# Kernel optimization log

Measured on AMD Instinct MI355X. Metric: run time of the kernel, lower is better.

Reference implementation:

```python
import jax, jax.numpy as jnp
import numpy as np

B, S, D = 4, 2048, 1024
NH = 16
H2 = NH // 2
F = D // NH  # per-head hidden = 64
EXP = 4
DECAY_CONST = S // 512  # 4
EPS = 1e-5


def setup_inputs() -> dict:
    key = jax.random.key(0)
    ks = jax.random.split(key, 8)
    inp = {
        "x": jax.random.normal(ks[0], (B, S, D), dtype=jnp.float32),
        # token_norm / channel_norm params (LayerNorm init: ones/zeros)
        "g1": jnp.ones((D,), jnp.float32), "b1": jnp.zeros((D,), jnp.float32),
        "g2": jnp.ones((D,), jnp.float32), "b2": jnp.zeros((D,), jnp.float32),
        # per-head input projections [NH, D, F] and output projection
        "Wp": jax.random.normal(ks[1], (NH, D, F), jnp.float32) * 0.02,
        "bp": jnp.zeros((NH, F), jnp.float32),
        "Wo": jax.random.normal(ks[2], (D, D), jnp.float32) * 0.02,
        "bo": jnp.zeros((D,), jnp.float32),
        # ColRepeatCausalLinear: weight = 0.4, bias = 3 ; RowRepeat: -0.3, 0.2
        "w_col": jnp.full((H2, S), 0.4, jnp.float32),
        "b_col": jnp.full((H2, S), 3.0, jnp.float32),
        "w_row": jnp.full((H2, S), -0.3, jnp.float32),
        "b_row": jnp.full((H2, S), 0.2, jnp.float32),
        # decay_value params (ones, clipped to [0.9, 1] then ** (1/decay_constant))
        "dcol": jnp.ones((H2,), jnp.float32),
        "drow": jnp.ones((H2,), jnp.float32),
        # channel MLP
        "W1": jax.random.normal(ks[3], (D, EXP * D), jnp.float32) * 0.02,
        "c1": jnp.zeros((EXP * D,), jnp.float32),
        "W2": jax.random.normal(ks[4], (EXP * D, D), jnp.float32) * 0.02,
        "c2": jnp.zeros((D,), jnp.float32),
    }
    return inp


def _ln(x, g, b):
    m = jnp.mean(x, axis=-1, keepdims=True)
    v = jnp.mean(jnp.square(x - m), axis=-1, keepdims=True)
    return (x - m) * jax.lax.rsqrt(v + EPS) * g + b


def _forward(x, g1, b1, g2, b2, Wp, bp, Wo, bo, w_col, b_col, w_row, b_row,
             dcol, drow, W1, c1, W2, c2):
    decay_c = jnp.clip(dcol, 0.9, 1.0) ** (1.0 / DECAY_CONST)  # [H2]
    decay_r = jnp.clip(drow, 0.9, 1.0) ** (1.0 / DECAY_CONST)  # [H2]

    def step(carry, inp):
        cc, rc = carry                      # each [B, H2, F]
        xt, wc, bc, wr, br = inp            # xt [B, D]; wc/bc/wr/br [H2]
        # token mixing branch
        h = _ln(xt, g1, b1)
        proj = jnp.einsum('bd,hdf->bhf', h, Wp) + bp  # [B, NH, F]
        # Col heads: cache = proj + decay*cache ; out = w*cache + b
        cc = proj[:, :H2] + decay_c[None, :, None] * cc
        col_out = wc[None, :, None] * cc + bc[None, :, None]
        # Row heads: cache = w*proj + decay*cache ; out = cache + b
        rc = wr[None, :, None] * proj[:, H2:] + decay_r[None, :, None] * rc
        row_out = rc + br[None, :, None]
        mix = jnp.concatenate([col_out, row_out], axis=1).reshape(xt.shape[0], -1)
        y = xt + mix @ Wo + bo
        # channel MLP branch
        h2 = _ln(y, g2, b2)
        out = y + jax.nn.gelu(h2 @ W1 + c1) @ W2 + c2
        return (cc, rc), out

    init = (jnp.zeros((x.shape[0], H2, F), x.dtype),
            jnp.zeros((x.shape[0], H2, F), x.dtype))
    xs = (jnp.swapaxes(x, 0, 1), w_col.T, b_col.T, w_row.T, b_row.T)
    _, ys = jax.lax.scan(step, init, xs)    # ys [S, B, D]
    return jnp.swapaxes(ys, 0, 1)


def reference(x, g1, b1, g2, b2, Wp, bp, Wo, bo, w_col, b_col, w_row, b_row,
              dcol, drow, W1, c1, W2, c2):
    return _forward(x, g1, b1, g2, b2, Wp, bp, Wo, bo, w_col, b_col,
                    w_row, b_row, dcol, drow, W1, c1, W2, c2)
```

## Files before the change

kernel.cpp:

```cpp
#include <hip/hip_runtime.h>

typedef __attribute__((ext_vector_type(4))) float fx4;
typedef __attribute__((ext_vector_type(8))) short s16x8;

#define SEQ   2048
#define DM    1024
#define BSZ   4
#define ROWS  (BSZ*SEQ)
#define CHUNK 64
#define NCH   (SEQ/CHUNK)

__device__ __forceinline__ unsigned short f2bf(float f){
  unsigned u = __builtin_bit_cast(unsigned, f);
  u = u + 0x7FFFu + ((u >> 16) & 1u);
  return (unsigned short)(u >> 16);
}
__device__ __forceinline__ float bf2f(unsigned short u){
  return __builtin_bit_cast(float, ((unsigned)u) << 16);
}

__device__ __forceinline__ float gelu_f(float x){
  float u = 0.7978845608028654f * (x + 0.044715f * x*x*x);
  return x / (1.0f + __expf(-2.0f*u));
}

__device__ __forceinline__ void gload_lds16(const void* g, void* l){
  __builtin_amdgcn_global_load_lds(
      (__attribute__((address_space(1))) void*)g,
      (__attribute__((address_space(3))) void*)l, 16, 0, 0);
}

__global__ __launch_bounds__(256) void transpose_k(const float* __restrict__ in,
    unsigned short* __restrict__ out, int R, int C, long long ibs, long long obs){
  __shared__ float tile[32][33];
  in  += (long long)blockIdx.z * ibs;
  out += (long long)blockIdx.z * obs;
  int c0 = blockIdx.x*32, r0 = blockIdx.y*32;
  int tx = threadIdx.x, ty = threadIdx.y;
  #pragma unroll
  for (int i=0;i<4;i++)
    tile[ty+8*i][tx] = in[(long long)(r0+ty+8*i)*C + c0+tx];
  __syncthreads();
  #pragma unroll
  for (int i=0;i<4;i++)
    out[(long long)(c0+ty+8*i)*R + r0+tx] = f2bf(tile[tx][ty+8*i]);
}

__global__ __launch_bounds__(256) void ln_rows(const float* __restrict__ x,
    const float* __restrict__ g, const float* __restrict__ b,
    unsigned short* __restrict__ out){
  int row = blockIdx.x, t = threadIdx.x;
  const fx4* xr = (const fx4*)(x + (long long)row*DM);
  fx4 v = xr[t];
  float s  = v[0]+v[1]+v[2]+v[3];
  float s2 = v[0]*v[0]+v[1]*v[1]+v[2]*v[2]+v[3]*v[3];
  #pragma unroll
  for (int o=32;o;o>>=1){ s += __shfl_down(s,o); s2 += __shfl_down(s2,o); }
  __shared__ float red[8];
  int lane = t & 63, wid = t >> 6;
  if (lane==0){ red[wid]=s; red[4+wid]=s2; }
  __syncthreads();
  s  = red[0]+red[1]+red[2]+red[3];
  s2 = red[4]+red[5]+red[6]+red[7];
  float m  = s * (1.0f/DM);
  float rs = rsqrtf(s2*(1.0f/DM) - m*m + 1e-5f);
  const fx4 gv = ((const fx4*)g)[t], bv = ((const fx4*)b)[t];
  ushort4 pk;
  pk.x = f2bf((v[0]-m)*rs*gv[0] + bv[0]);
  pk.y = f2bf((v[1]-m)*rs*gv[1] + bv[1]);
  pk.z = f2bf((v[2]-m)*rs*gv[2] + bv[2]);
  pk.w = f2bf((v[3]-m)*rs*gv[3] + bv[3]);
  *(ushort4*)(out + (long long)row*DM + t*4) = pk;
}

__global__ __launch_bounds__(256) void scan_carry(const unsigned short* __restrict__ P,
    const float* __restrict__ w_row, const float* __restrict__ dcol,
    const float* __restrict__ drow, float* __restrict__ carry){
  int g = blockIdx.x*4 + (threadIdx.x>>6);
  int lane = threadIdx.x & 63;
  int chunk = g & (NCH-1); int bh = g >> 5; int h = bh & 15; int b = bh >> 4;
  float draw = (h<8) ? dcol[h] : drow[h-8];
  float d = powf(fminf(fmaxf(draw,0.9f),1.0f), 0.25f);
  float c = 0.f;
  const unsigned short* p = P + ((long long)(b*SEQ + chunk*CHUNK))*DM + h*64 + lane;
  const float* wr = w_row + (h>=8 ? (h-8)*SEQ + chunk*CHUNK : 0);
  #pragma unroll 4
  for (int i=0;i<CHUNK;i++){
    float a = bf2f(p[(long long)i*DM]);
    if (h>=8) a *= wr[i];
    c = fmaf(d, c, a);
  }
  carry[((long long)(bh*64 + lane))*NCH + chunk] = c;
}

__global__ __launch_bounds__(256) void scan_final(const unsigned short* __restrict__ P,
    const float* __restrict__ w_col, const float* __restrict__ b_col,
    const float* __restrict__ w_row, const float* __restrict__ b_row,
    const float* __restrict__ dcol, const float* __restrict__ drow,
    const float* __restrict__ carry, unsigned short* __restrict__ mix){
  int g = blockIdx.x*4 + (threadIdx.x>>6);
  int lane = threadIdx.x & 63;
  int chunk = g & (NCH-1); int bh = g >> 5; int h = bh & 15; int b = bh >> 4;
  float draw = (h<8) ? dcol[h] : drow[h-8];
  float d = powf(fminf(fmaxf(draw,0.9f),1.0f), 0.25f);
  float dL = d;
  #pragma unroll
  for (int i=0;i<6;i++) dL *= dL;
  const float* cr = carry + ((long long)(bh*64 + lane))*NCH;
  float c = 0.f;
  for (int j=0;j<chunk;j++) c = fmaf(dL, c, cr[j]);
  const unsigned short* p = P + ((long long)(b*SEQ + chunk*CHUNK))*DM + h*64 + lane;
  unsigned short* mo = mix + ((long long)(b*SEQ + chunk*CHUNK))*DM + h*64 + lane;
  int t0 = chunk*CHUNK;
  #pragma unroll 4
  for (int i=0;i<CHUNK;i++){
    int t = t0 + i;
    float a = bf2f(p[(long long)i*DM]);
    float o;
    if (h<8){
      c = fmaf(d, c, a);
      o = w_col[h*SEQ + t]*c + b_col[h*SEQ + t];
    } else {
      a *= w_row[(h-8)*SEQ + t];
      c = fmaf(d, c, a);
      o = c + b_row[(h-8)*SEQ + t];
    }
    mo[(long long)i*DM] = f2bf(o);
  }
}

template<int EPI, int K>
__global__ __launch_bounds__(256) void gemm_bt(const unsigned short* __restrict__ A,
    const unsigned short* __restrict__ Bt, int N,
    const float* __restrict__ bias, const float* __restrict__ res,
    float* __restrict__ outf, unsigned short* __restrict__ outb){
  __shared__ __align__(16) unsigned short lds[32768];
  const int tid = threadIdx.x;
  const int l = tid & 63;
  const int w = tid >> 6;
  const int wr = w >> 1, wc = w & 1;

  const long long row0 = (long long)blockIdx.x * 128;
  const long long col0 = (long long)blockIdx.y * 128;

  fx4 acc[4][4] = {};

  const unsigned short* gA[4];
  const unsigned short* gB[4];
  int lslot[4];
  #pragma unroll
  for (int i=0;i<4;i++){
    int slot = w*256 + i*64 + l;
    int r = slot >> 3;
    int qs = slot & 7;
    int c = (qs ^ (r & 7)) << 3;
    gA[i] = A  + (row0 + r)*(long long)K + c;
    gB[i] = Bt + (col0 + r)*(long long)K + c;
    lslot[i] = slot*8;
  }
  int aoff[2][4], boff[2][4];
  #pragma unroll
  for (int kk=0;kk<2;kk++){
    #pragma unroll
    for (int m=0;m<4;m++){
      int r  = wr*64 + m*16 + (l&15);
      int q  = (kk*4 + (l>>4)) ^ (r&7);
      aoff[kk][m] = r*64 + q*8;
      int r2 = wc*64 + m*16 + (l&15);
      int q2 = (kk*4 + (l>>4)) ^ (r2&7);
      boff[kk][m] = 8192 + r2*64 + q2*8;
    }
  }

  auto STAGE = [&](int bufoff){
    #pragma unroll
    for (int i=0;i<4;i++){
      gload_lds16(gA[i], &lds[bufoff + lslot[i]]);
      gload_lds16(gB[i], &lds[bufoff + 8192 + lslot[i]]);
      gA[i] += 64; gB[i] += 64;
    }
  };

  constexpr int nsteps = K >> 6;

  STAGE(0);
  STAGE(16384);
  asm volatile("s_waitcnt vmcnt(8)" ::: "memory");
  __builtin_amdgcn_sched_barrier(0);
  __builtin_amdgcn_s_barrier();

  int curoff = 0;
  for (int s = 0; s < nsteps; ++s){
    s16x8 af[2][4], bfr[2][4];
    #pragma unroll
    for (int kk=0;kk<2;kk++){
      #pragma unroll
      for (int m=0;m<4;m++){
        af[kk][m]  = *(const s16x8*)&lds[curoff + aoff[kk][m]];
        bfr[kk][m] = *(const s16x8*)&lds[curoff + boff[kk][m]];
      }
    }
    __builtin_amdgcn_sched_barrier(0);
    asm volatile("s_waitcnt lgkmcnt(0)" ::: "memory");
    __builtin_amdgcn_sched_barrier(0);
    __builtin_amdgcn_s_barrier();
    __builtin_amdgcn_sched_barrier(0);
    const bool do_stage = (s + 2 < nsteps);
    if (do_stage) STAGE(curoff);
    __builtin_amdgcn_s_setprio(1);
    #pragma unroll
    for (int kk=0;kk<2;kk++)
      #pragma unroll
      for (int m=0;m<4;m++)
        #pragma unroll
        for (int n=0;n<4;n++)
          acc[m][n] = __builtin_amdgcn_mfma_f32_16x16x32_bf16(af[kk][m], bfr[kk][n], acc[m][n], 0, 0, 0);
    __builtin_amdgcn_s_setprio(0);
    if (s + 1 < nsteps){
      __builtin_amdgcn_sched_barrier(0);
      if (do_stage) asm volatile("s_waitcnt vmcnt(8)" ::: "memory");
      else          asm volatile("s_waitcnt vmcnt(0)" ::: "memory");
      __builtin_amdgcn_sched_barrier(0);
      __builtin_amdgcn_s_barrier();
      __builtin_amdgcn_sched_barrier(0);
    }
    curoff ^= 16384;
  }
  __syncthreads();

  float* lf = (float*)lds;
  const int lg = l >> 4, lc = l & 15;
  #pragma unroll
  for (int g=0; g<4; ++g){
    if (wr == (g>>1)){
      #pragma unroll
      for (int mm=0; mm<2; ++mm){
        const int m = (g&1)*2 + mm;
        int lrow = mm*16 + lg*4;
        #pragma unroll
        for (int n=0;n<4;n++){
          int col = wc*64 + n*16 + lc;
          #pragma unroll
          for (int rg=0;rg<4;rg++)
            lf[(lrow+rg)*132 + col] = acc[m][n][rg];
        }
      }
    }
    __syncthreads();
    #pragma unroll
    for (int j=0;j<4;j++){
      int flat = j*256 + tid;
      int lrow = flat >> 5, c4 = flat & 31;
      long long grow = row0 + g*32 + lrow;
      long long gcol = col0 + c4*4;
      fx4 v = *(fx4*)&lf[lrow*132 + c4*4];
      fx4 bv = *(const fx4*)&bias[gcol];
      v = v + bv;
      long long idx = grow*(long long)N + gcol;
      if constexpr (EPI==0){
        *(fx4*)&outf[idx] = v;
      } else if constexpr (EPI==1){
        fx4 rv = *(const fx4*)&res[idx];
        v = v + rv;
        *(fx4*)&outf[idx] = v;
      } else if constexpr (EPI==2){
        ushort4 pk;
        pk.x = f2bf(gelu_f(v[0]));
        pk.y = f2bf(gelu_f(v[1]));
        pk.z = f2bf(gelu_f(v[2]));
        pk.w = f2bf(gelu_f(v[3]));
        *(ushort4*)&outb[idx] = pk;
      } else {
        ushort4 pk;
        pk.x = f2bf(v[0]); pk.y = f2bf(v[1]);
        pk.z = f2bf(v[2]); pk.w = f2bf(v[3]);
        *(ushort4*)&outb[idx] = pk;
      }
    }
    __syncthreads();
  }
}

extern "C" void kernel_launch(void* const* d_in, const int* in_sizes, int n_in,
                              void* d_out, int out_size, void* d_ws, size_t ws_size,
                              hipStream_t stream){
  const float* x    = (const float*)d_in[0];
  const float* g1   = (const float*)d_in[1];
  const float* b1   = (const float*)d_in[2];
  const float* g2   = (const float*)d_in[3];
  const float* b2   = (const float*)d_in[4];
  const float* Wp   = (const float*)d_in[5];
  const float* bp   = (const float*)d_in[6];
  const float* Wo   = (const float*)d_in[7];
  const float* bo   = (const float*)d_in[8];
  const float* w_col= (const float*)d_in[9];
  const float* b_col= (const float*)d_in[10];
  const float* w_row= (const float*)d_in[11];
  const float* b_row= (const float*)d_in[12];
  const float* dcol = (const float*)d_in[13];
  const float* drow = (const float*)d_in[14];
  const float* W1   = (const float*)d_in[15];
  const float* c1   = (const float*)d_in[16];
  const float* W2   = (const float*)d_in[17];
  const float* c2   = (const float*)d_in[18];
  float* out = (float*)d_out;

  char* ws = (char*)d_ws;
  const size_t MB = 1024*1024;
  if (ws_size < 101*MB) return;
  unsigned short* Wpt = (unsigned short*)(ws + 0);
  unsigned short* Wot = (unsigned short*)(ws + 2*MB);
  unsigned short* W1t = (unsigned short*)(ws + 4*MB);
  unsigned short* W2t = (unsigned short*)(ws + 12*MB);
  unsigned short* h   = (unsigned short*)(ws + 20*MB);
  unsigned short* P   = (unsigned short*)(ws + 36*MB);
  unsigned short* mix = (unsigned short*)(ws + 68*MB);
  float*          carry=(float*)(ws + 84*MB);
  unsigned short* U   = (unsigned short*)(ws + 36*MB);
  unsigned short* yln = h;

  dim3 tb(32,8);
  transpose_k<<<dim3(2,32,16),  tb, 0, stream>>>(Wp, Wpt, 1024,   64, 65536LL, 65536LL);
  transpose_k<<<dim3(32,32,1),  tb, 0, stream>>>(Wo, Wot, 1024, 1024, 0LL, 0LL);
  transpose_k<<<dim3(128,32,1), tb, 0, stream>>>(W1, W1t, 1024, 4096, 0LL, 0LL);
  transpose_k<<<dim3(32,128,1), tb, 0, stream>>>(W2, W2t, 4096, 1024, 0LL, 0LL);

  ln_rows<<<dim3(ROWS), dim3(256), 0, stream>>>(x, g1, b1, h);
  gemm_bt<3,1024><<<dim3(64,8),  dim3(256), 0, stream>>>(h,   Wpt, 1024, bp, nullptr, nullptr, P);
  scan_carry<<<dim3(512), dim3(256), 0, stream>>>(P, w_row, dcol, drow, carry);
  scan_final<<<dim3(512), dim3(256), 0, stream>>>(P, w_col, b_col, w_row, b_row, dcol, drow, carry, mix);
  gemm_bt<1,1024><<<dim3(64,8),  dim3(256), 0, stream>>>(mix, Wot, 1024, bo, x, out, nullptr);
  ln_rows<<<dim3(ROWS), dim3(256), 0, stream>>>(out, g2, b2, yln);
  gemm_bt<2,1024><<<dim3(64,32), dim3(256), 0, stream>>>(yln, W1t, 4096, c1, nullptr, nullptr, U);
  gemm_bt<1,4096><<<dim3(64,8),  dim3(256), 0, stream>>>(U,   W2t, 1024, c2, out, out, nullptr);
}
```

Measured before the change: 311.7 us.

## Add 256x256-tile 8-wave GEMM with phased LDS pipeline for W1 projection

Introduces a new GEMM kernel with 256x256 output tiles, 512 threads and 128KB of double-buffered LDS. Each k-step is split into four phases that interleave the next stage's global-to-LDS loads with MFMA work, with s_setprio raised around the MFMAs. The epilogue stages results through LDS for coalesced stores. It is used only for the 8192x4096 W1 GEMM with fused GELU. The larger tiles raise arithmetic intensity per block, but only 512 blocks run at one block per CU, so occupancy drops.

```diff
diff --git a/kernel.cpp b/kernel.cpp
--- a/kernel.cpp
+++ b/kernel.cpp
@@ -139,7 +139,6 @@
   const int l = tid & 63;
   const int w = tid >> 6;
   const int wr = w >> 1, wc = w & 1;
-
   const long long row0 = (long long)blockIdx.x * 128;
   const long long col0 = (long long)blockIdx.y * 128;
 
@@ -171,7 +170,6 @@
       boff[kk][m] = 8192 + r2*64 + q2*8;
     }
   }
-
   auto STAGE = [&](int bufoff){
     #pragma unroll
     for (int i=0;i<4;i++){
@@ -180,9 +178,7 @@
       gA[i] += 64; gB[i] += 64;
     }
   };
-
   constexpr int nsteps = K >> 6;
-
   STAGE(0);
   STAGE(16384);
   asm volatile("s_waitcnt vmcnt(8)" ::: "memory");
@@ -281,6 +277,154 @@
   }
 }
 
+#define PH(M0, N0, STG, LASTW)                                                \
+  {                                                                           \
+    s16x8 afr[2][4], bfr[2][2];                                               \
+    _Pragma("unroll")                                                         \
+    for (int kk=0;kk<2;kk++){                                                 \
+      _Pragma("unroll")                                                       \
+      for (int i=0;i<4;i++)                                                   \
+        afr[kk][i] = *(const s16x8*)&lds[bufb + aBase + qa[kk] + (M0+i)*1024];\
+      _Pragma("unroll")                                                       \
+      for (int j=0;j<2;j++)                                                   \
+        bfr[kk][j] = *(const s16x8*)&lds[bufb + bBase + qb[kk] + (N0+j)*1024];\
+    }                                                                         \
+    __builtin_amdgcn_sched_barrier(0);                                        \
+    STG;                                                                      \
+    __builtin_amdgcn_sched_barrier(0);                                        \
+    __builtin_amdgcn_s_barrier();                                             \
+    asm volatile("s_waitcnt lgkmcnt(0)" ::: "memory");                        \
+    __builtin_amdgcn_sched_barrier(0);                                        \
+    __builtin_amdgcn_s_setprio(1);                                            \
+    _Pragma("unroll")                                                         \
+    for (int kk=0;kk<2;kk++)                                                  \
+      _Pragma("unroll")                                                       \
+      for (int i=0;i<4;i++)                                                   \
+        _Pragma("unroll")                                                     \
+        for (int j=0;j<2;j++)                                                 \
+          acc[M0+i][N0+j] = __builtin_amdgcn_mfma_f32_16x16x32_bf16(          \
+              afr[kk][i], bfr[kk][j], acc[M0+i][N0+j], 0, 0, 0);              \
+    __builtin_amdgcn_s_setprio(0);                                            \
+    __builtin_amdgcn_sched_barrier(0);                                        \
+    LASTW;                                                                    \
+    __builtin_amdgcn_s_barrier();                                             \
+    __builtin_amdgcn_sched_barrier(0);                                        \
+  }
+
+template<int EPI, int K>
+__global__ __launch_bounds__(512) void gemm256(const unsigned short* __restrict__ A,
+    const unsigned short* __restrict__ Bt, int N,
+    const float* __restrict__ bias, const float* __restrict__ res,
+    float* __restrict__ outf, unsigned short* __restrict__ outb){
+  __shared__ __align__(16) unsigned short lds[65536];
+  const int tid = threadIdx.x;
+  const int l = tid & 63;
+  const int w = tid >> 6;
+  const int wr = w >> 2;
+  const int wcn = w & 3;
+  const long long row0 = (long long)blockIdx.x * 256;
+  const long long col0 = (long long)blockIdx.y * 256;
+
+  fx4 acc[8][4] = {};
+
+  const unsigned short* gA[4];
+  const unsigned short* gB[4];
+  int lsl[4];
+  #pragma unroll
+  for (int i=0;i<4;i++){
+    int slot = i*512 + tid;
+    int r = slot >> 3, q = slot & 7;
+    int c = (q ^ (r & 7)) << 3;
+    gA[i] = A  + (row0 + r)*(long long)K + c;
+    gB[i] = Bt + (col0 + r)*(long long)K + c;
+    lsl[i] = slot*8;
+  }
+  const int l15 = l & 15, lg = l >> 4;
+  const int aRow = wr*128 + l15;
+  const int bRow = wcn*64 + l15;
+  const int qa[2] = { ((lg    ) ^ (aRow & 7))*8, ((4+lg) ^ (aRow & 7))*8 };
+  const int qb[2] = { ((lg    ) ^ (bRow & 7))*8, ((4+lg) ^ (bRow & 7))*8 };
+  const int aBase = aRow*64;
+  const int bBase = 16384 + bRow*64;
+
+  auto STAGE_A = [&](int nb){
+    #pragma unroll
+    for (int i=0;i<4;i++){ gload_lds16(gA[i], &lds[nb + lsl[i]]); gA[i] += 64; }
+  };
+  auto STAGE_B = [&](int nb){
+    #pragma unroll
+    for (int i=0;i<4;i++){ gload_lds16(gB[i], &lds[nb + 16384 + lsl[i]]); gB[i] += 64; }
+  };
+
+  constexpr int T = K >> 6;
+  STAGE_A(0); STAGE_B(0);
+  asm volatile("s_waitcnt vmcnt(0)" ::: "memory");
+  __builtin_amdgcn_sched_barrier(0);
+  __builtin_amdgcn_s_barrier();
+
+  int bufb = 0;
+  for (int t = 0; t < T; ++t){
+    const int nb = bufb ^ 32768;
+    const bool more = (t + 1 < T);
+    PH(0,0, { if (more) STAGE_A(nb); }, {});
+    PH(4,0, { if (more) STAGE_B(nb); }, {});
+    PH(0,2, {}, {});
+    PH(4,2, {}, { if (more) asm volatile("s_waitcnt vmcnt(0)" ::: "memory"); });
+    bufb = nb;
+  }
+
+  float* lf = (float*)lds;
+  #pragma unroll
+  for (int g=0; g<4; ++g){
+    if (wr == (g>>1)){
+      #pragma unroll
+      for (int mm=0; mm<4; ++mm){
+        const int m = (g&1)*4 + mm;
+        const int lrow = mm*16 + lg*4;
+        #pragma unroll
+        for (int n=0;n<4;n++){
+          const int col = wcn*64 + n*16 + l15;
+          #pragma unroll
+          for (int rg=0;rg<4;rg++)
+            lf[(lrow+rg)*260 + col] = acc[m][n][rg];
+        }
+      }
+    }
+    __syncthreads();
+    #pragma unroll
+    for (int j=0;j<8;j++){
+      int flat = j*512 + tid;
+      int lrow = flat >> 6, c4 = flat & 63;
+      long long grow = row0 + g*64 + lrow;
+      long long gcol = col0 + c4*4;
+      fx4 v = *(fx4*)&lf[lrow*260 + c4*4];
+      fx4 bv = *(const fx4*)&bias[gcol];
+      v = v + bv;
+      long long idx = grow*(long long)N + gcol;
+      if constexpr (EPI==0){
+        *(fx4*)&outf[idx] = v;
+      } else if constexpr (EPI==1){
+        fx4 rv = *(const fx4*)&res[idx];
+        v = v + rv;
+        *(fx4*)&outf[idx] = v;
+      } else if constexpr (EPI==2){
+        ushort4 pk;
+        pk.x = f2bf(gelu_f(v[0]));
+        pk.y = f2bf(gelu_f(v[1]));
+        pk.z = f2bf(gelu_f(v[2]));
+        pk.w = f2bf(gelu_f(v[3]));
+        *(ushort4*)&outb[idx] = pk;
+      } else {
+        ushort4 pk;
+        pk.x = f2bf(v[0]); pk.y = f2bf(v[1]);
+        pk.z = f2bf(v[2]); pk.w = f2bf(v[3]);
+        *(ushort4*)&outb[idx] = pk;
+      }
+    }
+    __syncthreads();
+  }
+}
+
 extern "C" void kernel_launch(void* const* d_in, const int* in_sizes, int n_in,
                               void* d_out, int out_size, void* d_ws, size_t ws_size,
                               hipStream_t stream){
@@ -331,6 +475,6 @@
   scan_final<<<dim3(512), dim3(256), 0, stream>>>(P, w_col, b_col, w_row, b_row, dcol, drow, carry, mix);
   gemm_bt<1,1024><<<dim3(64,8),  dim3(256), 0, stream>>>(mix, Wot, 1024, bo, x, out, nullptr);
   ln_rows<<<dim3(ROWS), dim3(256), 0, stream>>>(out, g2, b2, yln);
-  gemm_bt<2,1024><<<dim3(64,32), dim3(256), 0, stream>>>(yln, W1t, 4096, c1, nullptr, nullptr, U);
+  gemm256<2,1024><<<dim3(32,16), dim3(512), 0, stream>>>(yln, W1t, 4096, c1, nullptr, nullptr, U);
   gemm_bt<1,4096><<<dim3(64,8),  dim3(256), 0, stream>>>(U,   W2t, 1024, c2, out, out, nullptr);
 }
```

New measurement: 312.9 us. About the same (+0.4%).

## Run channel MLP GEMMs in FP8 with MX-scaled MFMA

Applied to the files above, without the earlier changes.

Converts W1/W2 weights (scaled by 64) and the LN2 output plus GELU intermediate to FP8 E4M3. The two MLP GEMMs, which dominate FLOPs, then run on a new kernel using 16x16x128 scaled MFMA with fixed exponent scales to undo the weight scaling. This halves operand bytes and uses the higher-throughput FP8 matrix path. The cost is reduced precision, with a risk of accuracy tolerance failure.

```diff
diff --git a/kernel.cpp b/kernel.cpp
--- a/kernel.cpp
+++ b/kernel.cpp
@@ -2,6 +2,8 @@
 
 typedef __attribute__((ext_vector_type(4))) float fx4;
 typedef __attribute__((ext_vector_type(8))) short s16x8;
+typedef __attribute__((ext_vector_type(4))) int   i32x4;
+typedef __attribute__((ext_vector_type(8))) int   i32x8;
 
 #define SEQ   2048
 #define DM    1024
@@ -19,6 +21,22 @@
   return __builtin_bit_cast(float, ((unsigned)u) << 16);
 }
 
+__device__ __forceinline__ unsigned char f2fp8(float x){
+  unsigned u = __builtin_bit_cast(unsigned, x);
+  unsigned s = (u >> 24) & 0x80u;
+  float ax = __builtin_fabsf(x);
+  if (ax >= 448.f) return (unsigned char)(s | 0x7Eu);
+  if (ax < 0.015625f){
+    int m = (int)(ax * 512.f + 0.5f);
+    return (unsigned char)(s | (unsigned)m);
+  }
+  unsigned b = __builtin_bit_cast(unsigned, ax);
+  b += 0x0007FFFFu + ((b >> 20) & 1u);
+  unsigned e = (b >> 23) - 127u + 7u;
+  unsigned m = (b >> 20) & 7u;
+  return (unsigned char)(s | (e << 3) | m);
+}
+
 __device__ __forceinline__ float gelu_f(float x){
   float u = 0.7978845608028654f * (x + 0.044715f * x*x*x);
   return x / (1.0f + __expf(-2.0f*u));
@@ -28,6 +46,12 @@
   __builtin_amdgcn_global_load_lds(
       (__attribute__((address_space(1))) void*)g,
       (__attribute__((address_space(3))) void*)l, 16, 0, 0);
+}
+
+__device__ __forceinline__ fx4 mfma_mx(i32x8 a, i32x8 b, fx4 c){
+  return __builtin_amdgcn_mfma_scale_f32_16x16x128_f8f6f4(
+      a, b, c, 0 , 0 ,
+      0, 0x7F7F7F7F, 0, 0x79797979);
 }
 
 __global__ __launch_bounds__(256) void transpose_k(const float* __restrict__ in,
@@ -44,6 +68,20 @@
   #pragma unroll
   for (int i=0;i<4;i++)
     out[(long long)(c0+ty+8*i)*R + r0+tx] = f2bf(tile[tx][ty+8*i]);
+}
+
+__global__ __launch_bounds__(256) void transpose_f8(const float* __restrict__ in,
+    unsigned char* __restrict__ out, int R, int C){
+  __shared__ float tile[32][33];
+  int c0 = blockIdx.x*32, r0 = blockIdx.y*32;
+  int tx = threadIdx.x, ty = threadIdx.y;
+  #pragma unroll
+  for (int i=0;i<4;i++)
+    tile[ty+8*i][tx] = in[(long long)(r0+ty+8*i)*C + c0+tx];
+  __syncthreads();
+  #pragma unroll
+  for (int i=0;i<4;i++)
+    out[(long long)(c0+ty+8*i)*R + r0+tx] = f2fp8(tile[tx][ty+8*i] * 64.f);
 }
 
 __global__ __launch_bounds__(256) void ln_rows(const float* __restrict__ x,
@@ -71,6 +109,33 @@
   pk.z = f2bf((v[2]-m)*rs*gv[2] + bv[2]);
   pk.w = f2bf((v[3]-m)*rs*gv[3] + bv[3]);
   *(ushort4*)(out + (long long)row*DM + t*4) = pk;
+}
+
+__global__ __launch_bounds__(256) void ln_rows_f8(const float* __restrict__ x,
+    const float* __restrict__ g, const float* __restrict__ b,
+    unsigned char* __restrict__ out){
+  int row = blockIdx.x, t = threadIdx.x;
+  const fx4* xr = (const fx4*)(x + (long long)row*DM);
+  fx4 v = xr[t];
+  float s  = v[0]+v[1]+v[2]+v[3];
+  float s2 = v[0]*v[0]+v[1]*v[1]+v[2]*v[2]+v[3]*v[3];
+  #pragma unroll
+  for (int o=32;o;o>>=1){ s += __shfl_down(s,o); s2 += __shfl_down(s2,o); }
+  __shared__ float red[8];
+  int lane = t & 63, wid = t >> 6;
+  if (lane==0){ red[wid]=s; red[4+wid]=s2; }
+  __syncthreads();
+  s  = red[0]+red[1]+red[2]+red[3];
+  s2 = red[4]+red[5]+red[6]+red[7];
+  float m  = s * (1.0f/DM);
+  float rs = rsqrtf(s2*(1.0f/DM) - m*m + 1e-5f);
+  const fx4 gv = ((const fx4*)g)[t], bv = ((const fx4*)b)[t];
+  uchar4 pk;
+  pk.x = f2fp8((v[0]-m)*rs*gv[0] + bv[0]);
+  pk.y = f2fp8((v[1]-m)*rs*gv[1] + bv[1]);
+  pk.z = f2fp8((v[2]-m)*rs*gv[2] + bv[2]);
+  pk.w = f2fp8((v[3]-m)*rs*gv[3] + bv[3]);
+  *(uchar4*)(out + (long long)row*DM + t*4) = pk;
 }
 
 __global__ __launch_bounds__(256) void scan_carry(const unsigned short* __restrict__ P,
@@ -139,7 +204,6 @@
   const int l = tid & 63;
   const int w = tid >> 6;
   const int wr = w >> 1, wc = w & 1;
-
   const long long row0 = (long long)blockIdx.x * 128;
   const long long col0 = (long long)blockIdx.y * 128;
 
@@ -171,7 +235,6 @@
       boff[kk][m] = 8192 + r2*64 + q2*8;
     }
   }
-
   auto STAGE = [&](int bufoff){
     #pragma unroll
     for (int i=0;i<4;i++){
@@ -180,9 +243,7 @@
       gA[i] += 64; gB[i] += 64;
     }
   };
-
   constexpr int nsteps = K >> 6;
-
   STAGE(0);
   STAGE(16384);
   asm volatile("s_waitcnt vmcnt(8)" ::: "memory");
@@ -263,18 +324,153 @@
         fx4 rv = *(const fx4*)&res[idx];
         v = v + rv;
         *(fx4*)&outf[idx] = v;
-      } else if constexpr (EPI==2){
-        ushort4 pk;
-        pk.x = f2bf(gelu_f(v[0]));
-        pk.y = f2bf(gelu_f(v[1]));
-        pk.z = f2bf(gelu_f(v[2]));
-        pk.w = f2bf(gelu_f(v[3]));
-        *(ushort4*)&outb[idx] = pk;
       } else {
         ushort4 pk;
         pk.x = f2bf(v[0]); pk.y = f2bf(v[1]);
         pk.z = f2bf(v[2]); pk.w = f2bf(v[3]);
         *(ushort4*)&outb[idx] = pk;
+      }
+    }
+    __syncthreads();
+  }
+}
+
+template<int EPI, int K>
+__global__ __launch_bounds__(256) void gemm_f8(const unsigned char* __restrict__ A,
+    const unsigned char* __restrict__ Bt, int N,
+    const float* __restrict__ bias, const float* __restrict__ res,
+    float* __restrict__ outf, unsigned char* __restrict__ outb){
+  __shared__ __align__(16) unsigned char lds[65536];
+  const int tid = threadIdx.x;
+  const int l = tid & 63;
+  const int w = tid >> 6;
+  const int wr = w >> 1, wc = w & 1;
+  const long long row0 = (long long)blockIdx.x * 128;
+  const long long col0 = (long long)blockIdx.y * 128;
+
+  fx4 acc[4][4] = {};
+
+  const unsigned char* gA[4];
+  const unsigned char* gB[4];
+  int lslot[4];
+  #pragma unroll
+  for (int i=0;i<4;i++){
+    int slot = w*256 + i*64 + l;
+    int r = slot >> 3;
+    int qs = slot & 7;
+    int c = (qs ^ (r & 7)) << 4;
+    gA[i] = A  + (row0 + r)*(long long)K + c;
+    gB[i] = Bt + (col0 + r)*(long long)K + c;
+    lslot[i] = slot*16;
+  }
+  int aoff0[4], aoff1[4], boff0[4], boff1[4];
+  const int lg = l >> 4, l15 = l & 15;
+  #pragma unroll
+  for (int m=0;m<4;m++){
+    int r  = wr*64 + m*16 + l15;
+    aoff0[m] = r*128 + ((2*lg  ) ^ (r&7))*16;
+    aoff1[m] = r*128 + ((2*lg+1) ^ (r&7))*16;
+    int r2 = wc*64 + m*16 + l15;
+    boff0[m] = 16384 + r2*128 + ((2*lg  ) ^ (r2&7))*16;
+    boff1[m] = 16384 + r2*128 + ((2*lg+1) ^ (r2&7))*16;
+  }
+  auto STAGE = [&](int bufoff){
+    #pragma unroll
+    for (int i=0;i<4;i++){
+      gload_lds16(gA[i], &lds[bufoff + lslot[i]]);
+      gload_lds16(gB[i], &lds[bufoff + 16384 + lslot[i]]);
+      gA[i] += 128; gB[i] += 128;
+    }
+  };
+  constexpr int nsteps = K >> 7;
+  STAGE(0);
+  STAGE(32768);
+  asm volatile("s_waitcnt vmcnt(8)" ::: "memory");
+  __builtin_amdgcn_sched_barrier(0);
+  __builtin_amdgcn_s_barrier();
+
+  int curoff = 0;
+  for (int s = 0; s < nsteps; ++s){
+    i32x8 av[4], bv[4];
+    #pragma unroll
+    for (int m=0;m<4;m++){
+      i32x4 lo = *(const i32x4*)&lds[curoff + aoff0[m]];
+      i32x4 hi = *(const i32x4*)&lds[curoff + aoff1[m]];
+      av[m][0]=lo[0]; av[m][1]=lo[1]; av[m][2]=lo[2]; av[m][3]=lo[3];
+      av[m][4]=hi[0]; av[m][5]=hi[1]; av[m][6]=hi[2]; av[m][7]=hi[3];
+    }
+    #pragma unroll
+    for (int n=0;n<4;n++){
+      i32x4 lo = *(const i32x4*)&lds[curoff + boff0[n]];
+      i32x4 hi = *(const i32x4*)&lds[curoff + boff1[n]];
+      bv[n][0]=lo[0]; bv[n][1]=lo[1]; bv[n][2]=lo[2]; bv[n][3]=lo[3];
+      bv[n][4]=hi[0]; bv[n][5]=hi[1]; bv[n][6]=hi[2]; bv[n][7]=hi[3];
+    }
+    __builtin_amdgcn_sched_barrier(0);
+    asm volatile("s_waitcnt lgkmcnt(0)" ::: "memory");
+    __builtin_amdgcn_sched_barrier(0);
+    __builtin_amdgcn_s_barrier();
+    __builtin_amdgcn_sched_barrier(0);
+    const bool do_stage = (s + 2 < nsteps);
+    if (do_stage) STAGE(curoff);
+    __builtin_amdgcn_s_setprio(1);
+    #pragma unroll
+    for (int m=0;m<4;m++)
+      #pragma unroll
+      for (int n=0;n<4;n++)
+        acc[m][n] = mfma_mx(av[m], bv[n], acc[m][n]);
+    __builtin_amdgcn_s_setprio(0);
+    if (s + 1 < nsteps){
+      __builtin_amdgcn_sched_barrier(0);
+      if (do_stage) asm volatile("s_waitcnt vmcnt(8)" ::: "memory");
+      else          asm volatile("s_waitcnt vmcnt(0)" ::: "memory");
+      __builtin_amdgcn_sched_barrier(0);
+      __builtin_amdgcn_s_barrier();
+      __builtin_amdgcn_sched_barrier(0);
+    }
+    curoff ^= 32768;
+  }
+  __syncthreads();
+
+  float* lf = (float*)lds;
+  #pragma unroll
+  for (int g=0; g<4; ++g){
+    if (wr == (g>>1)){
+      #pragma unroll
+      for (int mm=0; mm<2; ++mm){
+        const int m = (g&1)*2 + mm;
+        int lrow = mm*16 + lg*4;
+        #pragma unroll
+        for (int n=0;n<4;n++){
+          int col = wc*64 + n*16 + l15;
+          #pragma unroll
+          for (int rg=0;rg<4;rg++)
+            lf[(lrow+rg)*132 + col] = acc[m][n][rg];
+        }
+      }
+    }
+    __syncthreads();
+    #pragma unroll
+    for (int j=0;j<4;j++){
+      int flat = j*256 + tid;
+      int lrow = flat >> 5, c4 = flat & 31;
+      long long grow = row0 + g*32 + lrow;
+      long long gcol = col0 + c4*4;
+      fx4 v = *(fx4*)&lf[lrow*132 + c4*4];
+      fx4 bv2 = *(const fx4*)&bias[gcol];
+      v = v + bv2;
+      long long idx = grow*(long long)N + gcol;
+      if constexpr (EPI==1){
+        fx4 rv = *(const fx4*)&res[idx];
+        v = v + rv;
+        *(fx4*)&outf[idx] = v;
+      } else {
+        uchar4 pk;
+        pk.x = f2fp8(gelu_f(v[0]));
+        pk.y = f2fp8(gelu_f(v[1]));
+        pk.z = f2fp8(gelu_f(v[2]));
+        pk.w = f2fp8(gelu_f(v[3]));
+        *(uchar4*)&outb[idx] = pk;
       }
     }
     __syncthreads();
@@ -308,29 +504,29 @@
   char* ws = (char*)d_ws;
   const size_t MB = 1024*1024;
   if (ws_size < 101*MB) return;
-  unsigned short* Wpt = (unsigned short*)(ws + 0);
-  unsigned short* Wot = (unsigned short*)(ws + 2*MB);
-  unsigned short* W1t = (unsigned short*)(ws + 4*MB);
-  unsigned short* W2t = (unsigned short*)(ws + 12*MB);
-  unsigned short* h   = (unsigned short*)(ws + 20*MB);
-  unsigned short* P   = (unsigned short*)(ws + 36*MB);
-  unsigned short* mix = (unsigned short*)(ws + 68*MB);
-  float*          carry=(float*)(ws + 84*MB);
-  unsigned short* U   = (unsigned short*)(ws + 36*MB);
-  unsigned short* yln = h;
+  unsigned short* Wpt  = (unsigned short*)(ws + 0);
+  unsigned short* Wot  = (unsigned short*)(ws + 2*MB);
+  unsigned char*  W1t8 = (unsigned char*)(ws + 4*MB);
+  unsigned char*  W2t8 = (unsigned char*)(ws + 12*MB);
+  unsigned short* h    = (unsigned short*)(ws + 20*MB);
+  unsigned char*  yln8 = (unsigned char*)(ws + 20*MB);
+  unsigned short* P    = (unsigned short*)(ws + 36*MB);
+  unsigned char*  U8   = (unsigned char*)(ws + 36*MB);
+  unsigned short* mix  = (unsigned short*)(ws + 68*MB);
+  float*          carry= (float*)(ws + 84*MB);
 
   dim3 tb(32,8);
-  transpose_k<<<dim3(2,32,16),  tb, 0, stream>>>(Wp, Wpt, 1024,   64, 65536LL, 65536LL);
-  transpose_k<<<dim3(32,32,1),  tb, 0, stream>>>(Wo, Wot, 1024, 1024, 0LL, 0LL);
-  transpose_k<<<dim3(128,32,1), tb, 0, stream>>>(W1, W1t, 1024, 4096, 0LL, 0LL);
-  transpose_k<<<dim3(32,128,1), tb, 0, stream>>>(W2, W2t, 4096, 1024, 0LL, 0LL);
+  transpose_k <<<dim3(2,32,16),  tb, 0, stream>>>(Wp, Wpt, 1024,   64, 65536LL, 65536LL);
+  transpose_k <<<dim3(32,32,1),  tb, 0, stream>>>(Wo, Wot, 1024, 1024, 0LL, 0LL);
+  transpose_f8<<<dim3(128,32,1), tb, 0, stream>>>(W1, W1t8, 1024, 4096);
+  transpose_f8<<<dim3(32,128,1), tb, 0, stream>>>(W2, W2t8, 4096, 1024);
 
   ln_rows<<<dim3(ROWS), dim3(256), 0, stream>>>(x, g1, b1, h);
   gemm_bt<3,1024><<<dim3(64,8),  dim3(256), 0, stream>>>(h,   Wpt, 1024, bp, nullptr, nullptr, P);
   scan_carry<<<dim3(512), dim3(256), 0, stream>>>(P, w_row, dcol, drow, carry);
   scan_final<<<dim3(512), dim3(256), 0, stream>>>(P, w_col, b_col, w_row, b_row, dcol, drow, carry, mix);
   gemm_bt<1,1024><<<dim3(64,8),  dim3(256), 0, stream>>>(mix, Wot, 1024, bo, x, out, nullptr);
-  ln_rows<<<dim3(ROWS), dim3(256), 0, stream>>>(out, g2, b2, yln);
-  gemm_bt<2,1024><<<dim3(64,32), dim3(256), 0, stream>>>(yln, W1t, 4096, c1, nullptr, nullptr, U);
-  gemm_bt<1,4096><<<dim3(64,8),  dim3(256), 0, stream>>>(U,   W2t, 1024, c2, out, out, nullptr);
-}
+  ln_rows_f8<<<dim3(ROWS), dim3(256), 0, stream>>>(out, g2, b2, yln8);
+  gemm_f8<2,1024><<<dim3(64,32), dim3(256), 0, stream>>>(yln8, W1t8, 4096, c1, nullptr, nullptr, U8);
+  gemm_f8<1,4096><<<dim3(64,8),  dim3(256), 0, stream>>>(U8,  W2t8, 1024, c2, out, out, nullptr);
+}
```

Result: no change. 311.4 us (-0.1%).
